# Kernel optimization log

Measured on AMD Instinct MI355X. Metric: run time of the kernel, lower is better.

## Reference

```python
import jax, jax.numpy as jnp
import numpy as np
from jax import lax

KS = 3  # kernel_size
N = KS * KS


def _conv2d(x, w, stride, pad):
    return lax.conv_general_dilated(
        x, w, window_strides=(stride, stride), padding=((pad, pad), (pad, pad)),
        dimension_numbers=("NCHW", "OIHW", "NCHW"))


def setup_inputs() -> dict:
    key = jax.random.key(0)
    k1, k2, k3 = jax.random.split(key, 3)
    b, c, h, w = 4, 64, 128, 128
    outc = 128
    feat = jax.random.normal(k1, (b, c, h, w), dtype=jnp.float32)
    # small init so predicted offsets stay in a realistic range
    w_p = jax.random.normal(k2, (2 * N, c, 3, 3), dtype=jnp.float32) * 0.01
    b_p = jnp.zeros((2 * N,), dtype=jnp.float32)
    w_conv = jax.random.normal(k3, (outc, c, KS, KS), dtype=jnp.float32) * 0.05
    b_conv = jnp.zeros((outc,), dtype=jnp.float32)
    return {"feat": feat, "w_p": w_p, "b_p": b_p, "w_conv": w_conv, "b_conv": b_conv}


def _dcn_forward(feat, w_p, b_p, w_conv, b_conv):
    b, c, H, W = feat.shape
    # offset prediction: 3x3 conv, pad 1, stride 1 -> (b, 2N, h, w)
    offset = _conv2d(feat, w_p, 1, 1) + b_p[None, :, None, None]
    h, w = offset.shape[2], offset.shape[3]

    # p_n: kernel-relative offsets, meshgrid 'ij' (x block then y block)
    r = jnp.arange(-(KS - 1) // 2, (KS - 1) // 2 + 1)
    pnx, pny = jnp.meshgrid(r, r, indexing="ij")
    p_n = jnp.concatenate([pnx.ravel(), pny.ravel()]).reshape(1, 2 * N, 1, 1)
    # p_0: base sampling grid, starts at 1 (faithful to original)
    p0x, p0y = jnp.meshgrid(jnp.arange(1, h + 1), jnp.arange(1, w + 1), indexing="ij")
    p_0 = jnp.concatenate([
        jnp.broadcast_to(p0x.reshape(1, 1, h, w), (1, N, h, w)),
        jnp.broadcast_to(p0y.reshape(1, 1, h, w), (1, N, h, w)),
    ], axis=1)

    p = (p_0 + p_n).astype(offset.dtype) + offset          # (b, 2N, h, w)
    p = p.transpose(0, 2, 3, 1)                             # (b, h, w, 2N)

    q = jnp.floor(lax.stop_gradient(p))
    qltx = jnp.clip(q[..., :N], 0, H - 1).astype(jnp.int32)
    qlty = jnp.clip(q[..., N:], 0, W - 1).astype(jnp.int32)
    qrbx = jnp.clip(q[..., :N] + 1, 0, H - 1).astype(jnp.int32)
    qrby = jnp.clip(q[..., N:] + 1, 0, W - 1).astype(jnp.int32)

    px = jnp.clip(p[..., :N], 0, H - 1)
    py = jnp.clip(p[..., N:], 0, W - 1)

    fx_lt = qltx.astype(px.dtype); fy_lt = qlty.astype(py.dtype)
    fx_rb = qrbx.astype(px.dtype); fy_rb = qrby.astype(py.dtype)
    g_lt = (1 + (fx_lt - px)) * (1 + (fy_lt - py))
    g_rb = (1 - (fx_rb - px)) * (1 - (fy_rb - py))
    g_lb = (1 + (fx_lt - px)) * (1 - (fy_rb - py))  # q_lb = (lt_x, rb_y)
    g_rt = (1 - (fx_rb - px)) * (1 + (fy_lt - py))  # q_rt = (rb_x, lt_y)

    flat = feat.reshape(b, c, H * W)

    def gather(qx, qy):
        idx = (qx * W + qy).reshape(b, -1)               # (b, h*w*N)
        out = jax.vmap(lambda f, i: f[:, i])(flat, idx)  # (b, c, h*w*N)
        return out.reshape(b, c, h, w, N)

    x_off = (g_lt[:, None] * gather(qltx, qlty)
             + g_rb[:, None] * gather(qrbx, qrby)
             + g_lb[:, None] * gather(qltx, qrby)
             + g_rt[:, None] * gather(qrbx, qlty))        # (b, c, h, w, N)

    # N index = kx*KS + ky; final conv with stride==KS on the tiled map is
    # a per-position contraction over (c, kx, ky)
    x_off = x_off.reshape(b, c, h, w, KS, KS)
    out = jnp.einsum("bchwxy,ocxy->bohw", x_off, w_conv) + b_conv[None, :, None, None]
    return out


def reference(feat, w_p, b_p, w_conv, b_conv):
    return _dcn_forward(feat, w_p, b_p, w_conv, b_conv)
```

## Files before the change

kernel.cpp:

```cpp
#include <hip/hip_runtime.h>
#include <hip/hip_bf16.h>

#define HH 128
#define WW 128
#define CC 64
#define OCC 128
#define NB 4
#define HW (HH * WW)

#define OFF_OFS 0
#define WPT_OFS 1179648
#define WT_OFS  1190016

__global__ void transpose_weights(const float* __restrict__ w_p,
                                  const float* __restrict__ w_conv,
                                  float* __restrict__ ws) {
    int idx = blockIdx.x * blockDim.x + threadIdx.x;
    if (idx < 10368) {
        int c = idx / 162;
        int r = idx % 162;
        int n = r / 9, tap = r % 9;
        ws[WPT_OFS + idx] = w_p[(n * CC + c) * 9 + tap];
    }
    int idx2 = idx - 10368;
    if (idx2 >= 0 && idx2 < 73728) {
        int ck = idx2 >> 7, o = idx2 & 127;
        ws[WT_OFS + idx2] = w_conv[o * 576 + ck];
    }
}

__global__ __launch_bounds__(256) void offset_conv(
        const float* __restrict__ feat,
        const float* __restrict__ b_p,
        const float* __restrict__ wpt,
        float* __restrict__ off) {
    __shared__ float red[4][18][64];

    int bid = blockIdx.x;
    int jh = bid & 1;
    int i  = (bid >> 1) & 127;
    int b  = bid >> 8;
    int tid = threadIdx.x;
    int lane = tid & 63;
    int w = tid >> 6;
    int j = jh * 64 + lane;
    int c0 = w * 16;

    float acc[18];
#pragma unroll
    for (int n = 0; n < 18; ++n) acc[n] = 0.f;

    const float* fb = feat + b * CC * HW;
    const bool im1 = (i > 0), ip1 = (i < HH - 1);
    const bool jm1 = (j > 0), jp1 = (j < WW - 1);

    for (int cc = 0; cc < 16; ++cc) {
        int c = c0 + cc;
        const float* fc = fb + c * HW + i * WW + j;
        float f0 = (im1 && jm1) ? fc[-WW - 1] : 0.f;
        float f1 = im1          ? fc[-WW]     : 0.f;
        float f2 = (im1 && jp1) ? fc[-WW + 1] : 0.f;
        float f3 = jm1          ? fc[-1]      : 0.f;
        float f4 =                fc[0];
        float f5 = jp1          ? fc[1]       : 0.f;
        float f6 = (ip1 && jm1) ? fc[WW - 1]  : 0.f;
        float f7 = ip1          ? fc[WW]      : 0.f;
        float f8 = (ip1 && jp1) ? fc[WW + 1]  : 0.f;
        const float* wr = wpt + c * 162;
#pragma unroll
        for (int n = 0; n < 18; ++n) {
            acc[n] = fmaf(f0, wr[n * 9 + 0], acc[n]);
            acc[n] = fmaf(f1, wr[n * 9 + 1], acc[n]);
            acc[n] = fmaf(f2, wr[n * 9 + 2], acc[n]);
            acc[n] = fmaf(f3, wr[n * 9 + 3], acc[n]);
            acc[n] = fmaf(f4, wr[n * 9 + 4], acc[n]);
            acc[n] = fmaf(f5, wr[n * 9 + 5], acc[n]);
            acc[n] = fmaf(f6, wr[n * 9 + 6], acc[n]);
            acc[n] = fmaf(f7, wr[n * 9 + 7], acc[n]);
            acc[n] = fmaf(f8, wr[n * 9 + 8], acc[n]);
        }
    }
#pragma unroll
    for (int n = 0; n < 18; ++n) red[w][n][lane] = acc[n];
    __syncthreads();

    for (int it = tid; it < 18 * 64; it += 256) {
        int n = it >> 6, jj = it & 63;
        float v = b_p[n] + red[0][n][jj] + red[1][n][jj]
                         + red[2][n][jj] + red[3][n][jj];
        off[(b * 18 + n) * HW + i * WW + jh * 64 + jj] = v;
    }
}

__global__ __launch_bounds__(256) void dcn_main(
        const float* __restrict__ feat,
        const float* __restrict__ b_conv,
        const float* __restrict__ off,
        const float* __restrict__ wt,
        float* __restrict__ out) {
    __shared__ unsigned int xsp[144 * 64];

    int bid = blockIdx.x;
    int jh = bid & 1;
    int i  = (bid >> 1) & 127;
    int b  = bid >> 8;
    int j0 = jh * 64;
    int tid = threadIdx.x;
    int lane = tid & 63;
    int wu = __builtin_amdgcn_readfirstlane(tid >> 6);
    int o0 = wu * 32;

    float acc[32];
#pragma unroll
    for (int oo = 0; oo < 32; ++oo) acc[oo] = 0.f;

    const float* fb = feat + b * CC * HW;
    unsigned short* xs16 = (unsigned short*)xsp;

    for (int h = 0; h < 2; ++h) {
        for (int item = tid; item < 576; item += 256) {
            int n = item >> 6;
            int pos = item & 63;
            int j = j0 + pos;
            int sp = i * WW + j;
            float offx = off[(b * 18 + n) * HW + sp];
            float offy = off[(b * 18 + 9 + n) * HW + sp];
            float px = (float)(i + (n / 3)) + offx;
            float py = (float)(j + (n % 3)) + offy;
            float qxf = floorf(px), qyf = floorf(py);
            int x0 = min(max((int)qxf, 0), HH - 1);
            int y0 = min(max((int)qyf, 0), WW - 1);
            int x1 = min(max((int)qxf + 1, 0), HH - 1);
            int y1 = min(max((int)qyf + 1, 0), WW - 1);
            float pxc = fminf(fmaxf(px, 0.f), (float)(HH - 1));
            float pyc = fminf(fmaxf(py, 0.f), (float)(WW - 1));
            float gx0 = 1.f + ((float)x0 - pxc);
            float gx1 = 1.f - ((float)x1 - pxc);
            float gy0 = 1.f + ((float)y0 - pyc);
            float gy1 = 1.f - ((float)y1 - pyc);
            float glt = gx0 * gy0, grb = gx1 * gy1;
            float glb = gx0 * gy1, grt = gx1 * gy0;
            int o00 = x0 * WW + y0, o11 = x1 * WW + y1;
            int o01 = x0 * WW + y1, o10 = x1 * WW + y0;
            const float* fc = fb + (h * 32) * HW;
#pragma unroll 4
            for (int cc = 0; cc < 32; ++cc) {
                float v = glt * fc[o00] + grb * fc[o11]
                        + glb * fc[o01] + grt * fc[o10];
                int ckl = cc * 9 + n;
                unsigned int bits = __float_as_uint(v);
                unsigned int r = bits + 0x7fffu + ((bits >> 16) & 1u);
                xs16[((ckl >> 1) * 64 + pos) * 2 + (ckl & 1)] =
                    (unsigned short)(r >> 16);
                fc += HW;
            }
        }
        __syncthreads();

        const float* wbase = wt + (h * 288) * 128 + o0;
        for (int ckp = 0; ckp < 144; ++ckp) {
            unsigned int u = xsp[ckp * 64 + lane];
            float x0 = __uint_as_float(u << 16);
            float x1 = __uint_as_float(u & 0xffff0000u);
            const float* w0 = wbase + (ckp * 2) * 128;
            const float* w1 = w0 + 128;
#pragma unroll
            for (int oo = 0; oo < 32; ++oo) {
                acc[oo] = fmaf(x0, w0[oo], acc[oo]);
                acc[oo] = fmaf(x1, w1[oo], acc[oo]);
            }
        }
        __syncthreads();
    }

#pragma unroll
    for (int oo = 0; oo < 32; ++oo) {
        int o = o0 + oo;
        out[((b * OCC + o) * HH + i) * WW + j0 + lane] = acc[oo] + b_conv[o];
    }
}

extern "C" void kernel_launch(void* const* d_in, const int* in_sizes, int n_in,
                              void* d_out, int out_size, void* d_ws, size_t ws_size,
                              hipStream_t stream) {
    const float* feat   = (const float*)d_in[0];
    const float* w_p    = (const float*)d_in[1];
    const float* b_p    = (const float*)d_in[2];
    const float* w_conv = (const float*)d_in[3];
    const float* b_conv = (const float*)d_in[4];
    float* out = (float*)d_out;
    float* ws  = (float*)d_ws;

    float* off = ws + OFF_OFS;
    float* wpt = ws + WPT_OFS;
    float* wt  = ws + WT_OFS;

    hipLaunchKernelGGL(transpose_weights, dim3(329), dim3(256), 0, stream,
                       w_p, w_conv, ws);
    hipLaunchKernelGGL(offset_conv, dim3(NB * 128 * 2), dim3(256), 0, stream,
                       feat, b_p, wpt, off);
    hipLaunchKernelGGL(dcn_main, dim3(NB * 128 * 2), dim3(256), 0, stream,
                       feat, b_conv, off, wt, out);
}
```

Measured before the change: 289.6 us.

## Restructure DCN main kernel into MFMA-style bf16 fragment layout with scalar FMAs

Converts conv weights to bf16 in a 16x16 tile fragment layout and stores gathered samples position-major in a padded LDS row, written with 16-byte stores. The contraction is reorganised into per-wave 2x4 tiles of 4x4 accumulators that read bf16x8 vectors from LDS and global memory. It still uses scalar fmaf instead of matrix instructions, so each step adds repeated bf16-to-float unpacking. Weight reads also stop being wave-uniform, and weights now lose precision by being rounded to bf16.

```diff
diff --git a/kernel.cpp b/kernel.cpp
--- a/kernel.cpp
+++ b/kernel.cpp
@@ -1,5 +1,4 @@
 #include <hip/hip_runtime.h>
-#include <hip/hip_bf16.h>
 
 #define HH 128
 #define WW 128
@@ -7,25 +6,46 @@
 #define OCC 128
 #define NB 4
 #define HW (HH * WW)
-
-#define OFF_OFS 0
-#define WPT_OFS 1179648
-#define WT_OFS  1190016
-
-__global__ void transpose_weights(const float* __restrict__ w_p,
-                                  const float* __restrict__ w_conv,
-                                  float* __restrict__ ws) {
-    int idx = blockIdx.x * blockDim.x + threadIdx.x;
-    if (idx < 10368) {
-        int c = idx / 162;
-        int r = idx % 162;
+#define ROWB 296
+
+typedef short bf16x8 __attribute__((ext_vector_type(8)));
+typedef float f32x4 __attribute__((ext_vector_type(4)));
+
+#define WAF_OFS_B 4718592
+#define WPT_OFS_B 4866048
+
+__device__ inline unsigned short tobf16(float v) {
+    unsigned int u = __float_as_uint(v);
+    u += 0x7fffu + ((u >> 16) & 1u);
+    return (unsigned short)(u >> 16);
+}
+__device__ inline float frombf16(unsigned short s) {
+    return __uint_as_float(((unsigned int)s) << 16);
+}
+__device__ inline unsigned int bf16pair(float a, float b) {
+    return (unsigned int)tobf16(a) | ((unsigned int)tobf16(b) << 16);
+}
+
+__global__ void prep_weights(const float* __restrict__ w_p,
+                             const float* __restrict__ w_conv,
+                             unsigned short* __restrict__ wAf,
+                             float* __restrict__ wpt) {
+    int idx = blockIdx.x * 256 + threadIdx.x;
+    if (idx < 73728) {
+        int e = idx & 7, l = (idx >> 3) & 63;
+        int q = idx >> 9;
+        int s = q % 9, q2 = q / 9;
+        int h = q2 & 1, t = q2 >> 1;
+        int o = t * 16 + (l & 15);
+        int c = h * 32 + ((l >> 4) << 3) + e;
+        wAf[idx] = tobf16(w_conv[(o * 64 + c) * 9 + s]);
+    }
+    int idx2 = idx - 73728;
+    if (idx2 >= 0 && idx2 < 10368) {
+        int c = idx2 / 162;
+        int r = idx2 % 162;
         int n = r / 9, tap = r % 9;
-        ws[WPT_OFS + idx] = w_p[(n * CC + c) * 9 + tap];
-    }
-    int idx2 = idx - 10368;
-    if (idx2 >= 0 && idx2 < 73728) {
-        int ck = idx2 >> 7, o = idx2 & 127;
-        ws[WT_OFS + idx2] = w_conv[o * 576 + ck];
+        wpt[idx2] = w_p[(n * CC + c) * 9 + tap];
     }
 }
 
@@ -96,37 +116,34 @@
         const float* __restrict__ feat,
         const float* __restrict__ b_conv,
         const float* __restrict__ off,
-        const float* __restrict__ wt,
+        const unsigned short* __restrict__ wAf,
         float* __restrict__ out) {
-    __shared__ unsigned int xsp[144 * 64];
+    __shared__ __align__(16) unsigned short xs[64 * ROWB];
 
     int bid = blockIdx.x;
-    int jh = bid & 1;
-    int i  = (bid >> 1) & 127;
-    int b  = bid >> 8;
+    int jh = bid & 1, i = (bid >> 1) & 127, b = bid >> 8;
     int j0 = jh * 64;
-    int tid = threadIdx.x;
-    int lane = tid & 63;
+    int tid = threadIdx.x, lane = tid & 63;
     int wu = __builtin_amdgcn_readfirstlane(tid >> 6);
-    int o0 = wu * 32;
-
-    float acc[32];
-#pragma unroll
-    for (int oo = 0; oo < 32; ++oo) acc[oo] = 0.f;
-
-    const float* fb = feat + b * CC * HW;
-    unsigned short* xs16 = (unsigned short*)xsp;
+
+    float acc[2][4][4];
+#pragma unroll
+    for (int tl = 0; tl < 2; ++tl)
+#pragma unroll
+        for (int nt = 0; nt < 4; ++nt)
+#pragma unroll
+            for (int r = 0; r < 4; ++r) acc[tl][nt][r] = 0.f;
+
+    int m16 = (lane >> 4) << 2;
 
     for (int h = 0; h < 2; ++h) {
         for (int item = tid; item < 576; item += 256) {
-            int n = item >> 6;
-            int pos = item & 63;
-            int j = j0 + pos;
-            int sp = i * WW + j;
+            int n = item >> 6, pos = item & 63;
+            int j = j0 + pos, sp = i * WW + j;
             float offx = off[(b * 18 + n) * HW + sp];
             float offy = off[(b * 18 + 9 + n) * HW + sp];
-            float px = (float)(i + (n / 3)) + offx;
-            float py = (float)(j + (n % 3)) + offy;
+            float px = (float)(i + n / 3) + offx;
+            float py = (float)(j + n % 3) + offy;
             float qxf = floorf(px), qyf = floorf(py);
             int x0 = min(max((int)qxf, 0), HH - 1);
             int y0 = min(max((int)qyf, 0), WW - 1);
@@ -142,42 +159,65 @@
             float glb = gx0 * gy1, grt = gx1 * gy0;
             int o00 = x0 * WW + y0, o11 = x1 * WW + y1;
             int o01 = x0 * WW + y1, o10 = x1 * WW + y0;
-            const float* fc = fb + (h * 32) * HW;
-#pragma unroll 4
-            for (int cc = 0; cc < 32; ++cc) {
-                float v = glt * fc[o00] + grb * fc[o11]
-                        + glb * fc[o01] + grt * fc[o10];
-                int ckl = cc * 9 + n;
-                unsigned int bits = __float_as_uint(v);
-                unsigned int r = bits + 0x7fffu + ((bits >> 16) & 1u);
-                xs16[((ckl >> 1) * 64 + pos) * 2 + (ckl & 1)] =
-                    (unsigned short)(r >> 16);
+            const float* fc = feat + (b * 64 + h * 32) * HW;
+            unsigned int pk[16];
+#pragma unroll
+            for (int p = 0; p < 16; ++p) {
+                float v0 = glt * fc[o00] + grb * fc[o11] + glb * fc[o01] + grt * fc[o10];
                 fc += HW;
+                float v1 = glt * fc[o00] + grb * fc[o11] + glb * fc[o01] + grt * fc[o10];
+                fc += HW;
+                pk[p] = bf16pair(v0, v1);
+            }
+            uint4* dst = (uint4*)&xs[pos * ROWB + n * 32];
+#pragma unroll
+            for (int q = 0; q < 4; ++q)
+                dst[q] = make_uint4(pk[4 * q], pk[4 * q + 1], pk[4 * q + 2], pk[4 * q + 3]);
+        }
+        __syncthreads();
+
+        for (int s = 0; s < 9; ++s) {
+#pragma unroll
+            for (int kg = 0; kg < 4; ++kg) {
+                bf16x8 xv[4];
+#pragma unroll
+                for (int nt = 0; nt < 4; ++nt)
+                    xv[nt] = *(const bf16x8*)
+                        &xs[(nt * 16 + (lane & 15)) * ROWB + s * 32 + kg * 8];
+#pragma unroll
+                for (int tl = 0; tl < 2; ++tl) {
+#pragma unroll
+                    for (int r = 0; r < 4; ++r) {
+                        int lp = kg * 16 + m16 + r;
+                        bf16x8 wv = *(const bf16x8*)
+                            &wAf[((((wu * 2 + tl) * 2 + h) * 9 + s) * 64 + lp) * 8];
+#pragma unroll
+                        for (int e = 0; e < 8; ++e) {
+                            float wf = frombf16((unsigned short)wv[e]);
+#pragma unroll
+                            for (int nt = 0; nt < 4; ++nt)
+                                acc[tl][nt][r] = fmaf(
+                                    wf, frombf16((unsigned short)xv[nt][e]),
+                                    acc[tl][nt][r]);
+                        }
+                    }
+                }
             }
         }
         __syncthreads();
-
-        const float* wbase = wt + (h * 288) * 128 + o0;
-        for (int ckp = 0; ckp < 144; ++ckp) {
-            unsigned int u = xsp[ckp * 64 + lane];
-            float x0 = __uint_as_float(u << 16);
-            float x1 = __uint_as_float(u & 0xffff0000u);
-            const float* w0 = wbase + (ckp * 2) * 128;
-            const float* w1 = w0 + 128;
-#pragma unroll
-            for (int oo = 0; oo < 32; ++oo) {
-                acc[oo] = fmaf(x0, w0[oo], acc[oo]);
-                acc[oo] = fmaf(x1, w1[oo], acc[oo]);
+    }
+
+#pragma unroll
+    for (int tl = 0; tl < 2; ++tl)
+#pragma unroll
+        for (int nt = 0; nt < 4; ++nt)
+#pragma unroll
+            for (int r = 0; r < 4; ++r) {
+                int o = (wu * 2 + tl) * 16 + m16 + r;
+                int pos = nt * 16 + (lane & 15);
+                out[((b * OCC + o) * HH + i) * WW + j0 + pos] =
+                    acc[tl][nt][r] + b_conv[o];
             }
-        }
-        __syncthreads();
-    }
-
-#pragma unroll
-    for (int oo = 0; oo < 32; ++oo) {
-        int o = o0 + oo;
-        out[((b * OCC + o) * HH + i) * WW + j0 + lane] = acc[oo] + b_conv[o];
-    }
 }
 
 extern "C" void kernel_launch(void* const* d_in, const int* in_sizes, int n_in,
@@ -189,16 +229,16 @@
     const float* w_conv = (const float*)d_in[3];
     const float* b_conv = (const float*)d_in[4];
     float* out = (float*)d_out;
-    float* ws  = (float*)d_ws;
-
-    float* off = ws + OFF_OFS;
-    float* wpt = ws + WPT_OFS;
-    float* wt  = ws + WT_OFS;
-
-    hipLaunchKernelGGL(transpose_weights, dim3(329), dim3(256), 0, stream,
-                       w_p, w_conv, ws);
+    char* ws   = (char*)d_ws;
+
+    float* off = (float*)ws;
+    unsigned short* wAf = (unsigned short*)(ws + WAF_OFS_B);
+    float* wpt          = (float*)(ws + WPT_OFS_B);
+
+    hipLaunchKernelGGL(prep_weights, dim3(329), dim3(256), 0, stream,
+                       w_p, w_conv, wAf, wpt);
     hipLaunchKernelGGL(offset_conv, dim3(NB * 128 * 2), dim3(256), 0, stream,
                        feat, b_p, wpt, off);
     hipLaunchKernelGGL(dcn_main, dim3(NB * 128 * 2), dim3(256), 0, stream,
-                       feat, b_conv, off, wt, out);
-}
+                       feat, b_conv, off, wAf, out);
+}
```

New measurement: 324.3 us. 1.12x slower.
